# Performance work log

Hardware: AMD Instinct MI355X
Metric: run time of the kernel (lower is better)

Reference implementation:

```python
import jax, jax.numpy as jnp
import numpy as np

HIDDEN = 1024
NUM_HEADS = 8
HEAD_DIM = HIDDEN // NUM_HEADS
MAX_BACKWARD = 11   # context_left - 1
MAX_FORWARD = 12    # context_right
SPAN = MAX_BACKWARD + MAX_FORWARD + 1  # 24

B, U, W, C = 8, 16, 128, 151


def setup_inputs() -> dict:
    key = jax.random.key(0)
    kq, kk, kp = jax.random.split(key, 3)
    queries = jax.random.normal(kq, (B, U, W, NUM_HEADS, HEAD_DIM), dtype=jnp.float32)
    keys = jax.random.normal(kk, (B, U, C, NUM_HEADS, HEAD_DIM), dtype=jnp.float32)
    # glorot-ish scale for pos_proj (hidden, num_heads*head_dim)
    pos_proj = jax.random.normal(kp, (HIDDEN, NUM_HEADS * HEAD_DIM), dtype=jnp.float32) * (1.0 / np.sqrt(HIDDEN))
    return {"queries": queries, "keys": keys, "pos_proj": pos_proj}


def _sinusoid_emb(pos_proj):
    # positions: max_backward .. -max_forward (descending), shape (SPAN,)
    pos = jnp.arange(MAX_BACKWARD, -(MAX_FORWARD + 1), -1, dtype=jnp.float32)
    num_ts = HIDDEN // 2
    inv_ts = jnp.ones((num_ts,), dtype=jnp.float32)  # module uses ones
    scaled = pos[:, None] * inv_ts[None, :]          # (SPAN, HIDDEN/2)
    signal = jnp.concatenate([jnp.sin(scaled), jnp.cos(scaled)], axis=-1)  # (SPAN, HIDDEN)
    proj = signal @ pos_proj                         # (SPAN, N*H)
    return proj.reshape(SPAN, NUM_HEADS, HEAD_DIM)


def _relative_shift(term_bd, context_size):
    # term_bd: (B, N, U, W, SPAN) -> (B, N, U, W, C)
    b, n, u, w, _ = term_bd.shape
    pad = context_size + 1 - SPAN
    padded = jnp.pad(term_bd, ((0, 0), (0, 0), (0, 0), (0, 0), (0, pad)))
    flat = padded.reshape(b, n, u, w * (context_size + 1))
    sliced = flat[:, :, :, : w * context_size]
    return sliced.reshape(b, n, u, w, context_size)


def reference(queries, keys, pos_proj):
    context_size = keys.shape[2]
    sin_emb = _sinusoid_emb(pos_proj)                      # (SPAN, N, H)
    qp = jnp.transpose(queries, (0, 3, 1, 2, 4))           # (B, N, U, W, H)
    kp = jnp.transpose(keys, (0, 3, 1, 4, 2))              # (B, N, U, H, C)
    term_ac = jnp.matmul(qp, kp)                           # (B, N, U, W, C)
    # term_bd: query-position interaction, (B, N, U, W, SPAN)
    term_bd = jnp.einsum("bnuwh,fnh->bnuwf", qp, sin_emb)
    term_bd = _relative_shift(term_bd, context_size)       # (B, N, U, W, C)
    return term_ac + term_bd
```

## Files before the change

### kernel.cpp

```cpp
#include <hip/hip_runtime.h>
#include <cmath>

#define NHEADS 8
#define HDIM 128
#define SPAN 24
#define U_ 16
#define W_ 128
#define C_ 151
#define HID 1024

typedef unsigned short ushort8v __attribute__((ext_vector_type(8)));
typedef unsigned short ushort4v __attribute__((ext_vector_type(4)));
typedef __bf16 bf16x8 __attribute__((ext_vector_type(8)));
typedef float f32x4 __attribute__((ext_vector_type(4)));

__device__ inline unsigned short f2bf(float f) {
    union { float f; unsigned u; } v; v.f = f;
    unsigned r = v.u + 0x7FFFu + ((v.u >> 16) & 1u);
    return (unsigned short)(r >> 16);
}
__device__ inline float bf2f(unsigned short u) {
    union { unsigned u; float f; } v; v.u = ((unsigned)u) << 16;
    return v.f;
}
__device__ inline ushort8v cvt8(float4 a, float4 b) {
    ushort8v v;
    v[0] = f2bf(a.x); v[1] = f2bf(a.y); v[2] = f2bf(a.z); v[3] = f2bf(a.w);
    v[4] = f2bf(b.x); v[5] = f2bf(b.y); v[6] = f2bf(b.z); v[7] = f2bf(b.w);
    return v;
}

__global__ void k_partial(const float* __restrict__ pp, float* __restrict__ part) {
    const int t = threadIdx.x;
    const int row0 = blockIdx.x * 16;
    float4 s = make_float4(0.f, 0.f, 0.f, 0.f);
    #pragma unroll
    for (int i = 0; i < 16; ++i) {
        float4 v = *(const float4*)(pp + (size_t)(row0 + i) * HID + t * 4);
        s.x += v.x; s.y += v.y; s.z += v.z; s.w += v.w;
    }
    *(float4*)(part + (size_t)blockIdx.x * HID + t * 4) = s;
}

struct SC { float s[SPAN]; float c[SPAN]; };

#define KEXT_BYTES (176 * 256)
#define BD_PITCH 25
#define AUX_OFF KEXT_BYTES
#define S12_OFF (KEXT_BYTES + 4096)

__global__ __launch_bounds__(512, 4) void k_main(const float* __restrict__ q,
                                                 const float* __restrict__ k,
                                                 const float* __restrict__ part,
                                                 float* __restrict__ out, SC sc) {
    __shared__ __align__(16) char lds_raw[KEXT_BYTES + W_ * BD_PITCH * 2];
    unsigned short* bd = (unsigned short*)(lds_raw + KEXT_BYTES);

    const int bid = blockIdx.x;
    const int n = bid & 7;
    const int u = (bid >> 3) & 15;
    const int b = bid >> 7;

    const size_t qbase = ((size_t)(b * U_ + u) * W_) * HID + n * HDIM;
    const size_t kbase = ((size_t)(b * U_ + u) * C_) * HID + n * HDIM;
    const size_t obase = ((size_t)((b * NHEADS + n) * U_ + u)) * (W_ * C_);

    const int tid = threadIdx.x;
    const int lane = tid & 63;
    const int wave = tid >> 6;
    const int w0 = wave * 16;
    const int lr = lane & 15;
    const int lk = lane >> 4;

    float4 pf0[5], pf1[5];
    #pragma unroll
    for (int it = 0; it < 5; ++it) {
        const int ui = it * 512 + tid;
        const int r = ui >> 4, u16 = ui & 15;
        if (r < C_) {
            const float* src = k + kbase + (size_t)r * HID + u16 * 8;
            pf0[it] = *(const float4*)src;
            pf1[it] = *(const float4*)(src + 4);
        }
    }
    const int c4 = tid & 31, rg = tid >> 5;
    float4 pp4[4];
    #pragma unroll
    for (int i = 0; i < 4; ++i)
        pp4[i] = *(const float4*)(part + (size_t)(rg * 4 + i) * HID + n * HDIM + c4 * 4);
    const float* qrow = q + qbase + (size_t)(w0 + lr) * HID + lk * 8;
    float4 qpf[8];
    #pragma unroll
    for (int kk = 0; kk < 4; ++kk) {
        qpf[2 * kk]     = *(const float4*)(qrow + kk * 32);
        qpf[2 * kk + 1] = *(const float4*)(qrow + kk * 32 + 4);
    }

    #pragma unroll
    for (int it = 0; it < 5; ++it) {
        const int ui = it * 512 + tid;
        const int r = ui >> 4, u16 = ui & 15;
        if (r < C_) {
            const int dst = r * 256 + ((u16 * 16) ^ ((r & 7) << 4));
            *(ushort8v*)(lds_raw + dst) = cvt8(pf0[it], pf1[it]);
        }
    }
    {
        float4 rs;
        rs.x = pp4[0].x + pp4[1].x + pp4[2].x + pp4[3].x;
        rs.y = pp4[0].y + pp4[1].y + pp4[2].y + pp4[3].y;
        rs.z = pp4[0].z + pp4[1].z + pp4[2].z + pp4[3].z;
        rs.w = pp4[0].w + pp4[1].w + pp4[2].w + pp4[3].w;
        ushort4v rb;
        rb[0] = f2bf(rs.x); rb[1] = f2bf(rs.y); rb[2] = f2bf(rs.z); rb[3] = f2bf(rs.w);
        *(ushort4v*)(lds_raw + AUX_OFF + rg * 256 + c4 * 8) = rb;
    }
    __syncthreads();

    if (tid < 256) {
        const int col = tid & 127, half = tid >> 7;
        float s = 0.f;
        #pragma unroll
        for (int g = 0; g < 8; ++g)
            s += bf2f(*(const unsigned short*)(lds_raw + AUX_OFF + (half * 8 + g) * 256 + col * 2));
        *(float*)(lds_raw + S12_OFF + (half * 128 + col) * 4) = s;
    }
    __syncthreads();

    if (tid < 384) {
        const int f = tid >> 4, u16 = tid & 15;
        const int r = C_ + f;
        const float sf = sc.s[f], cf = sc.c[f];
        ushort8v v;
        #pragma unroll
        for (int e = 0; e < 8; ++e) {
            const int col = u16 * 8 + e;
            const float S1 = *(const float*)(lds_raw + S12_OFF + col * 4);
            const float S2 = *(const float*)(lds_raw + S12_OFF + 512 + col * 4);
            v[e] = f2bf(sf * S1 + cf * S2);
        }
        const int dst = r * 256 + ((u16 * 16) ^ ((r & 7) << 4));
        *(ushort8v*)(lds_raw + dst) = v;
    } else if (tid < 400) {
        const int u16 = tid - 384, r = 175;
        const int dst = r * 256 + ((u16 * 16) ^ ((r & 7) << 4));
        *(ushort8v*)(lds_raw + dst) = (ushort8v)(unsigned short)0;
    }
    bf16x8 qf[4];
    #pragma unroll
    for (int kk = 0; kk < 4; ++kk)
        qf[kk] = __builtin_bit_cast(bf16x8, cvt8(qpf[2 * kk], qpf[2 * kk + 1]));

    __syncthreads();

    f32x4 acc[11];
    #pragma unroll
    for (int j = 0; j < 11; ++j) acc[j] = (f32x4)(0.f);

    #pragma unroll
    for (int kk = 0; kk < 4; ++kk) {
        #pragma unroll
        for (int j = 0; j < 11; ++j) {
            const int r = j * 16 + lr;
            const int byt = r * 256 + (((kk * 64) + (lk * 16)) ^ ((r & 7) << 4));
            bf16x8 bf = __builtin_bit_cast(bf16x8, *(const ushort8v*)(lds_raw + byt));
            acc[j] = __builtin_amdgcn_mfma_f32_16x16x32_bf16(qf[kk], bf, acc[j], 0, 0, 0);
        }
    }

    {
        const int c9 = 144 + lr;
        if (c9 >= C_) {
            const int f = c9 - C_;
            #pragma unroll
            for (int reg = 0; reg < 4; ++reg) {
                const int w = w0 + lk * 4 + reg;
                bd[w * BD_PITCH + f] = f2bf(acc[9][reg]);
            }
        }
        const int f10 = 9 + lr;
        if (f10 < SPAN) {
            #pragma unroll
            for (int reg = 0; reg < 4; ++reg) {
                const int w = w0 + lk * 4 + reg;
                bd[w * BD_PITCH + f10] = f2bf(acc[10][reg]);
            }
        }
    }

    #pragma unroll
    for (int j = 0; j < 10; ++j) {
        const int c = j * 16 + lr;
        if (c < C_) {
            #pragma unroll
            for (int reg = 0; reg < 4; ++reg) {
                const int w = w0 + lk * 4 + reg;
                float v = acc[j][reg];
                const int d = c - w;
                if (d >= 0 && d < SPAN) v += bf2f(bd[w * BD_PITCH + d]);
                out[obase + (size_t)w * C_ + c] = v;
            }
        }
    }
}

extern "C" void kernel_launch(void* const* d_in, const int* in_sizes, int n_in,
                              void* d_out, int out_size, void* d_ws, size_t ws_size,
                              hipStream_t stream) {
    const float* queries = (const float*)d_in[0];
    const float* keys    = (const float*)d_in[1];
    const float* posproj = (const float*)d_in[2];
    float* out = (float*)d_out;

    float* part = (float*)d_ws;

    SC sc;
    for (int f = 0; f < SPAN; ++f) {
        float p = (float)(11 - f);
        sc.s[f] = sinf(p);
        sc.c[f] = cosf(p);
    }

    k_partial<<<64, 256, 0, stream>>>(posproj, part);
    k_main<<<1024, 512, 0, stream>>>(queries, keys, part, out, sc);
}
```

Baseline: 50.90 us.

## Double-buffer key chunks in LDS to overlap global loads with MFMA

```diff
diff --git a/kernel.cpp b/kernel.cpp
--- a/kernel.cpp
+++ b/kernel.cpp
@@ -31,30 +31,114 @@
 }
 
 __global__ void k_partial(const float* __restrict__ pp, float* __restrict__ part) {
-    const int t = threadIdx.x;
-    const int row0 = blockIdx.x * 16;
+    const int bi = blockIdx.x >> 2, cj = blockIdx.x & 3;
+    const int col = cj * 256 + threadIdx.x * 4;
+    const int row0 = bi * 16;
     float4 s = make_float4(0.f, 0.f, 0.f, 0.f);
     #pragma unroll
     for (int i = 0; i < 16; ++i) {
-        float4 v = *(const float4*)(pp + (size_t)(row0 + i) * HID + t * 4);
+        float4 v = *(const float4*)(pp + (size_t)(row0 + i) * HID + col);
         s.x += v.x; s.y += v.y; s.z += v.z; s.w += v.w;
     }
-    *(float4*)(part + (size_t)blockIdx.x * HID + t * 4) = s;
+    *(float4*)(part + (size_t)bi * HID + col) = s;
 }
 
 struct SC { float s[SPAN]; float c[SPAN]; };
 
-#define KEXT_BYTES (176 * 256)
+#define CHUNK_B 8192
+#define AUX_OFF 16384
+#define S12_OFF (AUX_OFF + 4096)
 #define BD_PITCH 25
-#define AUX_OFF KEXT_BYTES
-#define S12_OFF (KEXT_BYTES + 4096)
+
+__device__ inline ushort8v emb8(const char* lds_raw, int f, int u16, const SC& sc) {
+    float4 s1a = *(const float4*)(lds_raw + S12_OFF + u16 * 32);
+    float4 s1b = *(const float4*)(lds_raw + S12_OFF + u16 * 32 + 16);
+    float4 s2a = *(const float4*)(lds_raw + S12_OFF + 512 + u16 * 32);
+    float4 s2b = *(const float4*)(lds_raw + S12_OFF + 512 + u16 * 32 + 16);
+    const float sf = sc.s[f], cf = sc.c[f];
+    ushort8v v;
+    v[0] = f2bf(sf * s1a.x + cf * s2a.x); v[1] = f2bf(sf * s1a.y + cf * s2a.y);
+    v[2] = f2bf(sf * s1a.z + cf * s2a.z); v[3] = f2bf(sf * s1a.w + cf * s2a.w);
+    v[4] = f2bf(sf * s1b.x + cf * s2b.x); v[5] = f2bf(sf * s1b.y + cf * s2b.y);
+    v[6] = f2bf(sf * s1b.z + cf * s2b.z); v[7] = f2bf(sf * s1b.w + cf * s2b.w);
+    return v;
+}
+
+#define ISSUE_K(c, P0, P1)                                                     \
+    {                                                                          \
+        const int r_ = 32 * (c) + (tid >> 4);                                  \
+        if (r_ < C_) {                                                         \
+            const float* s_ = k + kbase + (size_t)r_ * HID + u16 * 8;          \
+            P0 = *(const float4*)s_; P1 = *(const float4*)(s_ + 4);            \
+        }                                                                      \
+    }
+
+#define WRITE_PURE(c, P0, P1, BUFOFF)                                          \
+    {                                                                          \
+        const int rl_ = tid >> 4;                                              \
+        const int dst_ = (BUFOFF) + rl_ * 256 + ((u16 * 16) ^ ((rl_ & 7) << 4));\
+        *(ushort8v*)(lds_raw + dst_) = cvt8(P0, P1);                           \
+    }
+
+#define WRITE_C4(P0, P1, BUFOFF)                                               \
+    {                                                                          \
+        const int rl_ = tid >> 4;                                              \
+        const int r_ = 128 + rl_;                                              \
+        const int dst_ = (BUFOFF) + rl_ * 256 + ((u16 * 16) ^ ((rl_ & 7) << 4));\
+        ushort8v v_;                                                           \
+        if (r_ < C_) v_ = cvt8(P0, P1);                                        \
+        else         v_ = emb8(lds_raw, r_ - C_, u16, sc);                     \
+        *(ushort8v*)(lds_raw + dst_) = v_;                                     \
+    }
+
+#define WRITE_C5(BUFOFF)                                                       \
+    if (tid < 256) {                                                           \
+        const int rl_ = tid >> 4;                                              \
+        const int r_ = 160 + rl_;                                              \
+        const int dst_ = (BUFOFF) + rl_ * 256 + ((u16 * 16) ^ ((rl_ & 7) << 4));\
+        ushort8v v_;                                                           \
+        if (r_ < 175) v_ = emb8(lds_raw, r_ - C_, u16, sc);                    \
+        else          v_ = (ushort8v)(unsigned short)0;                        \
+        *(ushort8v*)(lds_raw + dst_) = v_;                                     \
+    }
+
+#define MFMA2(c, BUFOFF)                                                       \
+    {                                                                          \
+        _Pragma("unroll")                                                      \
+        for (int kk = 0; kk < 4; ++kk) {                                       \
+            _Pragma("unroll")                                                  \
+            for (int jj = 0; jj < 2; ++jj) {                                   \
+                const int rl = jj * 16 + lr;                                   \
+                const int byt = (BUFOFF) + rl * 256 +                          \
+                                (((kk * 64) + (lk * 16)) ^ ((rl & 7) << 4));   \
+                bf16x8 bf = __builtin_bit_cast(bf16x8,                         \
+                                *(const ushort8v*)(lds_raw + byt));            \
+                acc[2 * (c) + jj] = __builtin_amdgcn_mfma_f32_16x16x32_bf16(   \
+                                        qf[kk], bf, acc[2 * (c) + jj], 0, 0, 0);\
+            }                                                                  \
+        }                                                                      \
+    }
+
+#define MFMA1(BUFOFF)                                                          \
+    {                                                                          \
+        _Pragma("unroll")                                                      \
+        for (int kk = 0; kk < 4; ++kk) {                                       \
+            const int rl = lr;                                                 \
+            const int byt = (BUFOFF) + rl * 256 +                              \
+                            (((kk * 64) + (lk * 16)) ^ ((rl & 7) << 4));       \
+            bf16x8 bf = __builtin_bit_cast(bf16x8,                             \
+                            *(const ushort8v*)(lds_raw + byt));                \
+            acc[10] = __builtin_amdgcn_mfma_f32_16x16x32_bf16(                 \
+                          qf[kk], bf, acc[10], 0, 0, 0);                       \
+        }                                                                      \
+    }
 
 __global__ __launch_bounds__(512, 4) void k_main(const float* __restrict__ q,
                                                  const float* __restrict__ k,
                                                  const float* __restrict__ part,
                                                  float* __restrict__ out, SC sc) {
-    __shared__ __align__(16) char lds_raw[KEXT_BYTES + W_ * BD_PITCH * 2];
-    unsigned short* bd = (unsigned short*)(lds_raw + KEXT_BYTES);
+    __shared__ __align__(16) char lds_raw[AUX_OFF + W_ * BD_PITCH * 2];
+    unsigned short* bd = (unsigned short*)(lds_raw + AUX_OFF);
 
     const int bid = blockIdx.x;
     const int n = bid & 7;
@@ -71,23 +155,18 @@
     const int w0 = wave * 16;
     const int lr = lane & 15;
     const int lk = lane >> 4;
-
-    float4 pf0[5], pf1[5];
-    #pragma unroll
-    for (int it = 0; it < 5; ++it) {
-        const int ui = it * 512 + tid;
-        const int r = ui >> 4, u16 = ui & 15;
-        if (r < C_) {
-            const float* src = k + kbase + (size_t)r * HID + u16 * 8;
-            pf0[it] = *(const float4*)src;
-            pf1[it] = *(const float4*)(src + 4);
-        }
-    }
+    const int u16 = tid & 15;
+
     const int c4 = tid & 31, rg = tid >> 5;
     float4 pp4[4];
     #pragma unroll
     for (int i = 0; i < 4; ++i)
         pp4[i] = *(const float4*)(part + (size_t)(rg * 4 + i) * HID + n * HDIM + c4 * 4);
+
+    float4 a0, a1, b0, b1;
+    ISSUE_K(0, a0, a1);
+    ISSUE_K(1, b0, b1);
+
     const float* qrow = q + qbase + (size_t)(w0 + lr) * HID + lk * 8;
     float4 qpf[8];
     #pragma unroll
@@ -96,15 +175,6 @@
         qpf[2 * kk + 1] = *(const float4*)(qrow + kk * 32 + 4);
     }
 
-    #pragma unroll
-    for (int it = 0; it < 5; ++it) {
-        const int ui = it * 512 + tid;
-        const int r = ui >> 4, u16 = ui & 15;
-        if (r < C_) {
-            const int dst = r * 256 + ((u16 * 16) ^ ((r & 7) << 4));
-            *(ushort8v*)(lds_raw + dst) = cvt8(pf0[it], pf1[it]);
-        }
-    }
     {
         float4 rs;
         rs.x = pp4[0].x + pp4[1].x + pp4[2].x + pp4[3].x;
@@ -115,6 +185,7 @@
         rb[0] = f2bf(rs.x); rb[1] = f2bf(rs.y); rb[2] = f2bf(rs.z); rb[3] = f2bf(rs.w);
         *(ushort4v*)(lds_raw + AUX_OFF + rg * 256 + c4 * 8) = rb;
     }
+    WRITE_PURE(0, a0, a1, 0);
     __syncthreads();
 
     if (tid < 256) {
@@ -125,48 +196,28 @@
             s += bf2f(*(const unsigned short*)(lds_raw + AUX_OFF + (half * 8 + g) * 256 + col * 2));
         *(float*)(lds_raw + S12_OFF + (half * 128 + col) * 4) = s;
     }
-    __syncthreads();
-
-    if (tid < 384) {
-        const int f = tid >> 4, u16 = tid & 15;
-        const int r = C_ + f;
-        const float sf = sc.s[f], cf = sc.c[f];
-        ushort8v v;
-        #pragma unroll
-        for (int e = 0; e < 8; ++e) {
-            const int col = u16 * 8 + e;
-            const float S1 = *(const float*)(lds_raw + S12_OFF + col * 4);
-            const float S2 = *(const float*)(lds_raw + S12_OFF + 512 + col * 4);
-            v[e] = f2bf(sf * S1 + cf * S2);
-        }
-        const int dst = r * 256 + ((u16 * 16) ^ ((r & 7) << 4));
-        *(ushort8v*)(lds_raw + dst) = v;
-    } else if (tid < 400) {
-        const int u16 = tid - 384, r = 175;
-        const int dst = r * 256 + ((u16 * 16) ^ ((r & 7) << 4));
-        *(ushort8v*)(lds_raw + dst) = (ushort8v)(unsigned short)0;
-    }
     bf16x8 qf[4];
     #pragma unroll
     for (int kk = 0; kk < 4; ++kk)
         qf[kk] = __builtin_bit_cast(bf16x8, cvt8(qpf[2 * kk], qpf[2 * kk + 1]));
 
-    __syncthreads();
-
     f32x4 acc[11];
     #pragma unroll
     for (int j = 0; j < 11; ++j) acc[j] = (f32x4)(0.f);
 
-    #pragma unroll
-    for (int kk = 0; kk < 4; ++kk) {
-        #pragma unroll
-        for (int j = 0; j < 11; ++j) {
-            const int r = j * 16 + lr;
-            const int byt = r * 256 + (((kk * 64) + (lk * 16)) ^ ((r & 7) << 4));
-            bf16x8 bf = __builtin_bit_cast(bf16x8, *(const ushort8v*)(lds_raw + byt));
-            acc[j] = __builtin_amdgcn_mfma_f32_16x16x32_bf16(qf[kk], bf, acc[j], 0, 0, 0);
-        }
-    }
+    __syncthreads();
+
+    WRITE_PURE(1, b0, b1, CHUNK_B);  ISSUE_K(2, a0, a1);  MFMA2(0, 0);
+    __syncthreads();
+    WRITE_PURE(2, a0, a1, 0);        ISSUE_K(3, b0, b1);  MFMA2(1, CHUNK_B);
+    __syncthreads();
+    WRITE_PURE(3, b0, b1, CHUNK_B);  ISSUE_K(4, a0, a1);  MFMA2(2, 0);
+    __syncthreads();
+    WRITE_C4(a0, a1, 0);                                  MFMA2(3, CHUNK_B);
+    __syncthreads();
+    WRITE_C5(CHUNK_B);                                    MFMA2(4, 0);
+    __syncthreads();
+    MFMA1(CHUNK_B);
 
     {
         const int c9 = 144 + lr;
@@ -221,6 +272,6 @@
         sc.c[f] = cosf(p);
     }
 
-    k_partial<<<64, 256, 0, stream>>>(posproj, part);
+    k_partial<<<256, 64, 0, stream>>>(posproj, part);
     k_main<<<1024, 512, 0, stream>>>(queries, keys, part, out, sc);
 }
```

New measurement: 50.62 us. About the same (-0.5%).

## Load keys directly from global into MFMA operands instead of staging in LDS

Applied to the files above, without the earlier changes.

```diff
diff --git a/kernel.cpp b/kernel.cpp
--- a/kernel.cpp
+++ b/kernel.cpp
@@ -9,52 +9,74 @@
 #define C_ 151
 #define HID 1024
 
-typedef unsigned short ushort8v __attribute__((ext_vector_type(8)));
-typedef unsigned short ushort4v __attribute__((ext_vector_type(4)));
 typedef __bf16 bf16x8 __attribute__((ext_vector_type(8)));
 typedef float f32x4 __attribute__((ext_vector_type(4)));
 
-__device__ inline unsigned short f2bf(float f) {
-    union { float f; unsigned u; } v; v.f = f;
-    unsigned r = v.u + 0x7FFFu + ((v.u >> 16) & 1u);
-    return (unsigned short)(r >> 16);
-}
-__device__ inline float bf2f(unsigned short u) {
-    union { unsigned u; float f; } v; v.u = ((unsigned)u) << 16;
-    return v.f;
-}
-__device__ inline ushort8v cvt8(float4 a, float4 b) {
-    ushort8v v;
-    v[0] = f2bf(a.x); v[1] = f2bf(a.y); v[2] = f2bf(a.z); v[3] = f2bf(a.w);
-    v[4] = f2bf(b.x); v[5] = f2bf(b.y); v[6] = f2bf(b.z); v[7] = f2bf(b.w);
+__device__ inline bf16x8 mk8(float4 a, float4 b) {
+    bf16x8 v;
+    v[0] = (__bf16)a.x; v[1] = (__bf16)a.y; v[2] = (__bf16)a.z; v[3] = (__bf16)a.w;
+    v[4] = (__bf16)b.x; v[5] = (__bf16)b.y; v[6] = (__bf16)b.z; v[7] = (__bf16)b.w;
     return v;
 }
 
+#define BAR() asm volatile("s_waitcnt lgkmcnt(0)\n\ts_barrier" ::: "memory")
+
 __global__ void k_partial(const float* __restrict__ pp, float* __restrict__ part) {
-    const int t = threadIdx.x;
-    const int row0 = blockIdx.x * 16;
+    const int bi = blockIdx.x >> 2, cj = blockIdx.x & 3;
+    const int col = cj * 256 + threadIdx.x * 4;
+    const int row0 = bi * 16;
     float4 s = make_float4(0.f, 0.f, 0.f, 0.f);
     #pragma unroll
     for (int i = 0; i < 16; ++i) {
-        float4 v = *(const float4*)(pp + (size_t)(row0 + i) * HID + t * 4);
+        float4 v = *(const float4*)(pp + (size_t)(row0 + i) * HID + col);
         s.x += v.x; s.y += v.y; s.z += v.z; s.w += v.w;
     }
-    *(float4*)(part + (size_t)blockIdx.x * HID + t * 4) = s;
+    *(float4*)(part + (size_t)bi * HID + col) = s;
 }
 
 struct SC { float s[SPAN]; float c[SPAN]; };
 
-#define KEXT_BYTES (176 * 256)
+#define EMB_OFF 0
+#define REDP_OFF 6400
+#define S12_OFF 10496
+#define BD_OFF 11520
 #define BD_PITCH 25
-#define AUX_OFF KEXT_BYTES
-#define S12_OFF (KEXT_BYTES + 4096)
+
+__device__ inline bf16x8 emb8(const char* lds_raw, int f, int u16, const SC& sc) {
+    float4 s1a = *(const float4*)(lds_raw + S12_OFF + u16 * 32);
+    float4 s1b = *(const float4*)(lds_raw + S12_OFF + u16 * 32 + 16);
+    float4 s2a = *(const float4*)(lds_raw + S12_OFF + 512 + u16 * 32);
+    float4 s2b = *(const float4*)(lds_raw + S12_OFF + 512 + u16 * 32 + 16);
+    const float sf = sc.s[f], cf = sc.c[f];
+    bf16x8 v;
+    v[0] = (__bf16)(sf * s1a.x + cf * s2a.x); v[1] = (__bf16)(sf * s1a.y + cf * s2a.y);
+    v[2] = (__bf16)(sf * s1a.z + cf * s2a.z); v[3] = (__bf16)(sf * s1a.w + cf * s2a.w);
+    v[4] = (__bf16)(sf * s1b.x + cf * s2b.x); v[5] = (__bf16)(sf * s1b.y + cf * s2b.y);
+    v[6] = (__bf16)(sf * s1b.z + cf * s2b.z); v[7] = (__bf16)(sf * s1b.w + cf * s2b.w);
+    return v;
+}
+
+#define STORE_TILE(J)                                                          \
+    {                                                                          \
+        const int c_ = (J) * 16 + lr;                                          \
+        if (c_ < C_) {                                                         \
+            _Pragma("unroll")                                                  \
+            for (int reg = 0; reg < 4; ++reg) {                                \
+                const int w_ = w0 + lk * 4 + reg;                              \
+                float v_ = acc[J][reg];                                        \
+                const int d_ = c_ - w_;                                        \
+                if (d_ >= 0 && d_ < SPAN) v_ += (float)bd[w_ * BD_PITCH + d_]; \
+                out[obase + (size_t)w_ * C_ + c_] = v_;                        \
+            }                                                                  \
+        }                                                                      \
+    }
 
 __global__ __launch_bounds__(512, 4) void k_main(const float* __restrict__ q,
                                                  const float* __restrict__ k,
                                                  const float* __restrict__ part,
                                                  float* __restrict__ out, SC sc) {
-    __shared__ __align__(16) char lds_raw[KEXT_BYTES + W_ * BD_PITCH * 2];
-    unsigned short* bd = (unsigned short*)(lds_raw + KEXT_BYTES);
+    __shared__ __align__(16) char lds_raw[17920];
+    __bf16* bd = (__bf16*)(lds_raw + BD_OFF);
 
     const int bid = blockIdx.x;
     const int n = bid & 7;
@@ -72,22 +94,12 @@
     const int lr = lane & 15;
     const int lk = lane >> 4;
 
-    float4 pf0[5], pf1[5];
-    #pragma unroll
-    for (int it = 0; it < 5; ++it) {
-        const int ui = it * 512 + tid;
-        const int r = ui >> 4, u16 = ui & 15;
-        if (r < C_) {
-            const float* src = k + kbase + (size_t)r * HID + u16 * 8;
-            pf0[it] = *(const float4*)src;
-            pf1[it] = *(const float4*)(src + 4);
-        }
-    }
     const int c4 = tid & 31, rg = tid >> 5;
     float4 pp4[4];
     #pragma unroll
     for (int i = 0; i < 4; ++i)
         pp4[i] = *(const float4*)(part + (size_t)(rg * 4 + i) * HID + n * HDIM + c4 * 4);
+
     const float* qrow = q + qbase + (size_t)(w0 + lr) * HID + lk * 8;
     float4 qpf[8];
     #pragma unroll
@@ -96,75 +108,74 @@
         qpf[2 * kk + 1] = *(const float4*)(qrow + kk * 32 + 4);
     }
 
-    #pragma unroll
-    for (int it = 0; it < 5; ++it) {
-        const int ui = it * 512 + tid;
-        const int r = ui >> 4, u16 = ui & 15;
-        if (r < C_) {
-            const int dst = r * 256 + ((u16 * 16) ^ ((r & 7) << 4));
-            *(ushort8v*)(lds_raw + dst) = cvt8(pf0[it], pf1[it]);
-        }
-    }
     {
         float4 rs;
         rs.x = pp4[0].x + pp4[1].x + pp4[2].x + pp4[3].x;
         rs.y = pp4[0].y + pp4[1].y + pp4[2].y + pp4[3].y;
         rs.z = pp4[0].z + pp4[1].z + pp4[2].z + pp4[3].z;
         rs.w = pp4[0].w + pp4[1].w + pp4[2].w + pp4[3].w;
-        ushort4v rb;
-        rb[0] = f2bf(rs.x); rb[1] = f2bf(rs.y); rb[2] = f2bf(rs.z); rb[3] = f2bf(rs.w);
-        *(ushort4v*)(lds_raw + AUX_OFF + rg * 256 + c4 * 8) = rb;
-    }
-    __syncthreads();
+        __bf16* rp = (__bf16*)(lds_raw + REDP_OFF) + rg * 128 + c4 * 4;
+        rp[0] = (__bf16)rs.x; rp[1] = (__bf16)rs.y; rp[2] = (__bf16)rs.z; rp[3] = (__bf16)rs.w;
+    }
+    BAR();
 
     if (tid < 256) {
         const int col = tid & 127, half = tid >> 7;
+        const __bf16* rp = (const __bf16*)(lds_raw + REDP_OFF);
         float s = 0.f;
         #pragma unroll
-        for (int g = 0; g < 8; ++g)
-            s += bf2f(*(const unsigned short*)(lds_raw + AUX_OFF + (half * 8 + g) * 256 + col * 2));
+        for (int g = 0; g < 8; ++g) s += (float)rp[(half * 8 + g) * 128 + col];
         *(float*)(lds_raw + S12_OFF + (half * 128 + col) * 4) = s;
     }
-    __syncthreads();
-
-    if (tid < 384) {
-        const int f = tid >> 4, u16 = tid & 15;
-        const int r = C_ + f;
-        const float sf = sc.s[f], cf = sc.c[f];
-        ushort8v v;
-        #pragma unroll
-        for (int e = 0; e < 8; ++e) {
-            const int col = u16 * 8 + e;
-            const float S1 = *(const float*)(lds_raw + S12_OFF + col * 4);
-            const float S2 = *(const float*)(lds_raw + S12_OFF + 512 + col * 4);
-            v[e] = f2bf(sf * S1 + cf * S2);
-        }
-        const int dst = r * 256 + ((u16 * 16) ^ ((r & 7) << 4));
-        *(ushort8v*)(lds_raw + dst) = v;
-    } else if (tid < 400) {
-        const int u16 = tid - 384, r = 175;
-        const int dst = r * 256 + ((u16 * 16) ^ ((r & 7) << 4));
-        *(ushort8v*)(lds_raw + dst) = (ushort8v)(unsigned short)0;
-    }
     bf16x8 qf[4];
     #pragma unroll
     for (int kk = 0; kk < 4; ++kk)
-        qf[kk] = __builtin_bit_cast(bf16x8, cvt8(qpf[2 * kk], qpf[2 * kk + 1]));
-
-    __syncthreads();
+        qf[kk] = mk8(qpf[2 * kk], qpf[2 * kk + 1]);
+    BAR();
+
+    {
+        const int u16s = tid & 15;
+        if (tid < 384) {
+            const int e = tid >> 4;
+            bf16x8 v = emb8(lds_raw, e, u16s, sc);
+            const int dst = EMB_OFF + e * 256 + ((u16s * 16) ^ ((e & 7) << 4));
+            *(bf16x8*)(lds_raw + dst) = v;
+        } else if (tid < 400) {
+            const int dst = EMB_OFF + 24 * 256 + (u16s * 16);
+            *(bf16x8*)(lds_raw + dst) = (bf16x8)(__bf16)0.f;
+        }
+    }
+    BAR();
 
     f32x4 acc[11];
     #pragma unroll
     for (int j = 0; j < 11; ++j) acc[j] = (f32x4)(0.f);
 
-    #pragma unroll
-    for (int kk = 0; kk < 4; ++kk) {
-        #pragma unroll
-        for (int j = 0; j < 11; ++j) {
-            const int r = j * 16 + lr;
-            const int byt = r * 256 + (((kk * 64) + (lk * 16)) ^ ((r & 7) << 4));
-            bf16x8 bf = __builtin_bit_cast(bf16x8, *(const ushort8v*)(lds_raw + byt));
-            acc[j] = __builtin_amdgcn_mfma_f32_16x16x32_bf16(qf[kk], bf, acc[j], 0, 0, 0);
+    {
+        const int r = 144 + lr;
+        const float* kr = k + kbase + (size_t)r * HID + lk * 8;
+        const int e = lr - 7;
+        #pragma unroll
+        for (int kk = 0; kk < 4; ++kk) {
+            bf16x8 bf;
+            if (r < C_) {
+                float4 t0 = *(const float4*)(kr + kk * 32);
+                float4 t1 = *(const float4*)(kr + kk * 32 + 4);
+                bf = mk8(t0, t1);
+            } else {
+                const int byt = EMB_OFF + e * 256 + (((kk * 64) + (lk * 16)) ^ ((e & 7) << 4));
+                bf = *(const bf16x8*)(lds_raw + byt);
+            }
+            acc[9] = __builtin_amdgcn_mfma_f32_16x16x32_bf16(qf[kk], bf, acc[9], 0, 0, 0);
+        }
+    }
+    {
+        const int e = 9 + lr;
+        #pragma unroll
+        for (int kk = 0; kk < 4; ++kk) {
+            const int byt = EMB_OFF + e * 256 + (((kk * 64) + (lk * 16)) ^ ((e & 7) << 4));
+            bf16x8 bf = *(const bf16x8*)(lds_raw + byt);
+            acc[10] = __builtin_amdgcn_mfma_f32_16x16x32_bf16(qf[kk], bf, acc[10], 0, 0, 0);
         }
     }
 
@@ -175,7 +186,7 @@
             #pragma unroll
             for (int reg = 0; reg < 4; ++reg) {
                 const int w = w0 + lk * 4 + reg;
-                bd[w * BD_PITCH + f] = f2bf(acc[9][reg]);
+                bd[w * BD_PITCH + f] = (__bf16)acc[9][reg];
             }
         }
         const int f10 = 9 + lr;
@@ -183,24 +194,24 @@
             #pragma unroll
             for (int reg = 0; reg < 4; ++reg) {
                 const int w = w0 + lk * 4 + reg;
-                bd[w * BD_PITCH + f10] = f2bf(acc[10][reg]);
+                bd[w * BD_PITCH + f10] = (__bf16)acc[10][reg];
             }
         }
     }
 
-    #pragma unroll
-    for (int j = 0; j < 10; ++j) {
-        const int c = j * 16 + lr;
-        if (c < C_) {
-            #pragma unroll
-            for (int reg = 0; reg < 4; ++reg) {
-                const int w = w0 + lk * 4 + reg;
-                float v = acc[j][reg];
-                const int d = c - w;
-                if (d >= 0 && d < SPAN) v += bf2f(bd[w * BD_PITCH + d]);
-                out[obase + (size_t)w * C_ + c] = v;
-            }
-        }
+    STORE_TILE(9);
+
+    #pragma unroll
+    for (int j = 0; j < 9; ++j) {
+        const int r = j * 16 + lr;
+        const float* kr = k + kbase + (size_t)r * HID + lk * 8;
+        #pragma unroll
+        for (int kk = 0; kk < 4; ++kk) {
+            float4 t0 = *(const float4*)(kr + kk * 32);
+            float4 t1 = *(const float4*)(kr + kk * 32 + 4);
+            acc[j] = __builtin_amdgcn_mfma_f32_16x16x32_bf16(qf[kk], mk8(t0, t1), acc[j], 0, 0, 0);
+        }
+        STORE_TILE(j);
     }
 }
 
@@ -221,6 +232,6 @@
         sc.c[f] = cosf(p);
     }
 
-    k_partial<<<64, 256, 0, stream>>>(posproj, part);
+    k_partial<<<256, 64, 0, stream>>>(posproj, part);
     k_main<<<1024, 512, 0, stream>>>(queries, keys, part, out, sc);
 }
```

After: 96.42 us. +89.4%, slower.
